# Performance work log

Measured on AMD Instinct MI355X. Metric: run time of the kernel, lower is better.

## Reference

```python
import jax, jax.numpy as jnp
import numpy as np

T, B, I, H, L = 512, 64, 1024, 1024, 2


def setup_inputs() -> dict:
    key = jax.random.key(0)
    ks = jax.random.split(key, 3)
    stdv = 1.0 / np.sqrt(H)
    x = jax.random.normal(ks[0], (T, B, I), dtype=jnp.float32)
    w_ih = jax.random.uniform(ks[1], (L, 4 * H, I), dtype=jnp.float32, minval=-stdv, maxval=stdv)
    w_hh = jax.random.uniform(ks[2], (L, 4 * H, H), dtype=jnp.float32, minval=-stdv, maxval=stdv)
    b_ih = jnp.zeros((L, 4 * H), dtype=jnp.float32)
    b_hh = jnp.zeros((L, 4 * H), dtype=jnp.float32)
    h0 = jnp.zeros((L, B, H), dtype=jnp.float32)
    c0 = jnp.zeros((L, B, H), dtype=jnp.float32)
    return {"x": x, "h0": h0, "c0": c0, "w_ih": w_ih, "w_hh": w_hh, "b_ih": b_ih, "b_hh": b_hh}


def _lstm_layer(seq, h, c, w_ih_l, w_hh_l, b_ih_l, b_hh_l):
    # in2hidden: one big GEMM over all timesteps, as in the torch code
    igates = jnp.einsum('tbi,gi->tbg', seq, w_ih_l) + b_ih_l  # (T, B, 4H)

    def step(carry, ig):
        h, c = carry
        gates = ig + h @ w_hh_l.T + b_hh_l          # (B, 4H)
        i_g, f_g, g_g, o_g = jnp.split(gates, 4, axis=-1)
        c = jax.nn.sigmoid(f_g) * c + jax.nn.sigmoid(i_g) * jnp.tanh(g_g)
        h = jax.nn.sigmoid(o_g) * jnp.tanh(c)
        return (h, c), h

    (hT, cT), out = jax.lax.scan(step, (h, c), igates)
    return out, hT, cT


def reference(x, h0, c0, w_ih, w_hh, b_ih, b_hh):
    out = x
    h_fin, c_fin = [], []
    for l in range(L):  # small fixed number of structurally distinct layers
        out, hT, cT = _lstm_layer(out, h0[l], c0[l], w_ih[l], w_hh[l], b_ih[l], b_hh[l])
        h_fin.append(hT)
        c_fin.append(cT)
    return out, jnp.stack(h_fin), jnp.stack(c_fin)
```

## Files before the change

### kernel.cpp

```cpp
#include <hip/hip_runtime.h>
#include <hip/hip_bf16.h>
#include <stdint.h>

#define T_STEPS 512
#define NBATCH 64
#define HID 1024
#define NGATE 4096
#define NLAYERS 2
#define BH (NBATCH * HID)
#define TBH (T_STEPS * NBATCH * HID)
#define WEL ((size_t)NLAYERS * NGATE * HID)
#define GBLK 128

typedef __attribute__((ext_vector_type(8))) short short8;
typedef __attribute__((ext_vector_type(4))) float f32x4;

__device__ __forceinline__ ushort f2bf(float f) {
  union { float f; uint32_t i; } u; u.f = f;
  return (ushort)((u.i + 0x7fffu + ((u.i >> 16) & 1u)) >> 16);
}
__device__ __forceinline__ void gll16(const void* g, void* l) {
  __builtin_amdgcn_global_load_lds(
      (const __attribute__((address_space(1))) unsigned int*)g,
      (__attribute__((address_space(3))) unsigned int*)l, 16, 0, 0);
}

#define ISSC(S, P, OFF) \
  asm volatile("global_load_dwordx4 %0, %1, off offset:" #OFF \
               : "=v"(fr[S]) : "v"(P));
#define VMW(N, SLOT) \
  asm volatile("s_waitcnt vmcnt(" #N ")" : "+v"(fr[SLOT]));
#define CON(SLOT, KC) { \
    const short8 b0v = *(const short8*)(bb0 + ((((KC) * 64) + kb) ^ bsw)); \
    const short8 b1v = *(const short8*)(bb1 + ((((KC) * 64) + kb) ^ bsw)); \
    accA = __builtin_amdgcn_mfma_f32_16x16x32_bf16(fr[SLOT], b0v, accA, 0, 0, 0); \
    accB = __builtin_amdgcn_mfma_f32_16x16x32_bf16(fr[SLOT], b1v, accB, 0, 0, 0); }

#define PIPE32(Pp, KB) \
  ISSC(0,Pp,0)    ISSC(1,Pp,64)   ISSC(2,Pp,128)  ISSC(3,Pp,192)  \
  ISSC(4,Pp,256)  ISSC(5,Pp,320)  ISSC(6,Pp,384)  ISSC(7,Pp,448)  \
  ISSC(8,Pp,512)  ISSC(9,Pp,576)  ISSC(10,Pp,640) ISSC(11,Pp,704) \
  ISSC(12,Pp,768) ISSC(13,Pp,832) ISSC(14,Pp,896) ISSC(15,Pp,960) \
  VMW(15,0)  CON(0,(KB)+0)   ISSC(0,Pp,1024)  \
  VMW(15,1)  CON(1,(KB)+1)   ISSC(1,Pp,1088)  \
  VMW(15,2)  CON(2,(KB)+2)   ISSC(2,Pp,1152)  \
  VMW(15,3)  CON(3,(KB)+3)   ISSC(3,Pp,1216)  \
  VMW(15,4)  CON(4,(KB)+4)   ISSC(4,Pp,1280)  \
  VMW(15,5)  CON(5,(KB)+5)   ISSC(5,Pp,1344)  \
  VMW(15,6)  CON(6,(KB)+6)   ISSC(6,Pp,1408)  \
  VMW(15,7)  CON(7,(KB)+7)   ISSC(7,Pp,1472)  \
  VMW(15,8)  CON(8,(KB)+8)   ISSC(8,Pp,1536)  \
  VMW(15,9)  CON(9,(KB)+9)   ISSC(9,Pp,1600)  \
  VMW(15,10) CON(10,(KB)+10) ISSC(10,Pp,1664) \
  VMW(15,11) CON(11,(KB)+11) ISSC(11,Pp,1728) \
  VMW(15,12) CON(12,(KB)+12) ISSC(12,Pp,1792) \
  VMW(15,13) CON(13,(KB)+13) ISSC(13,Pp,1856) \
  VMW(15,14) CON(14,(KB)+14) ISSC(14,Pp,1920) \
  VMW(15,15) CON(15,(KB)+15) ISSC(15,Pp,1984) \
  VMW(15,0)  CON(0,(KB)+16)  \
  VMW(14,1)  CON(1,(KB)+17)  \
  VMW(13,2)  CON(2,(KB)+18)  \
  VMW(12,3)  CON(3,(KB)+19)  \
  VMW(11,4)  CON(4,(KB)+20)  \
  VMW(10,5)  CON(5,(KB)+21)  \
  VMW(9,6)   CON(6,(KB)+22)  \
  VMW(8,7)   CON(7,(KB)+23)  \
  VMW(7,8)   CON(8,(KB)+24)  \
  VMW(6,9)   CON(9,(KB)+25)  \
  VMW(5,10)  CON(10,(KB)+26) \
  VMW(4,11)  CON(11,(KB)+27) \
  VMW(3,12)  CON(12,(KB)+28) \
  VMW(2,13)  CON(13,(KB)+29) \
  VMW(1,14)  CON(14,(KB)+30) \
  VMW(0,15)  CON(15,(KB)+31)

__global__ void k_f32_to_bf16(const float* __restrict__ in, ushort* __restrict__ out, int n) {
  int i = (blockIdx.x * blockDim.x + threadIdx.x) * 4;
  if (i >= n) return;
  const float4 v = *reinterpret_cast<const float4*>(in + i);
  ushort4 o; o.x = f2bf(v.x); o.y = f2bf(v.y); o.z = f2bf(v.z); o.w = f2bf(v.w);
  *reinterpret_cast<ushort4*>(out + i) = o;
}
__global__ void k_zero(int* p, int n) {
  int i = blockIdx.x * blockDim.x + threadIdx.x;
  if (i < n) p[i] = 0;
}

struct ScanP {
  const ushort* wih; const ushort* whh;
  const ushort* xb;  const ushort* hinit;
  ushort* h0r;
  ushort* h1r;
  const float* c0; const float* bi; const float* bh;
  float* out; int* bar;
};

__device__ __forceinline__ void garrive(int* gb, int stripe) {
  __syncthreads();
  if (threadIdx.x == 0)
    __hip_atomic_fetch_add(gb + stripe * 16, 1, __ATOMIC_RELAXED, __HIP_MEMORY_SCOPE_AGENT);
}
__device__ __forceinline__ void gwait(int* gb, int target, bool isRoot) {
  if (threadIdx.x == 0) {
    if (isRoot) {
      const int need = target * GBLK;
      for (;;) {
        int sum = 0;
#pragma unroll
        for (int i = 0; i < 16; ++i)
          sum += __hip_atomic_load(gb + i * 16, __ATOMIC_RELAXED, __HIP_MEMORY_SCOPE_AGENT);
        if (sum >= need) break;
        __builtin_amdgcn_s_sleep(1);
      }
      __hip_atomic_store(gb + 256, target, __ATOMIC_RELAXED, __HIP_MEMORY_SCOPE_AGENT);
    } else {
      while (__hip_atomic_load(gb + 256, __ATOMIC_RELAXED, __HIP_MEMORY_SCOPE_AGENT) < target)
        __builtin_amdgcn_s_sleep(2);
    }
  }
  __syncthreads();
  __builtin_amdgcn_sched_barrier(0);
}

__global__ __launch_bounds__(256, 1) void k_scan(ScanP p) {
  __shared__ __align__(16) ushort Wl[32 * 2048];
  __shared__ float glds[64 * 33];
  const int tid = threadIdx.x, wave = tid >> 6, lane = tid & 63;
  const bool isL1 = blockIdx.x >= 128;
  const int cb = isL1 ? (int)blockIdx.x - 128 : (int)blockIdx.x;
  const int j0 = cb * 8;
  const int stripe = cb & 15;
  const bool isRoot = (cb == 0);
  int* gb = p.bar + (isL1 ? 512 : 0);
  int* rel0 = p.bar + 256;

  const ushort* wihL = p.wih + (isL1 ? (size_t)NGATE * HID : 0);
  const ushort* whhL = p.whh + (isL1 ? (size_t)NGATE * HID : 0);
  for (int q = wave; q < 128; q += 4) {
    const int i = q >> 2, ch = q & 3;
    const ushort* base = (ch < 2) ? wihL : whhL;
    const int g = (i >> 3) * 1024 + j0 + (i & 7);
    gll16(base + (size_t)g * 1024 + (ch & 1) * 512 + (((lane * 16) ^ ((i & 7) << 4)) >> 1),
          (char*)Wl + i * 4096 + ch * 1024);
  }

  const int eb  = tid >> 2;
  const int jl0 = (tid & 3) * 2;
  const int jj  = j0 + jl0;
  const int lofs = isL1 ? NGATE : 0;
  float creg[2], bias[4][2];
#pragma unroll
  for (int i = 0; i < 2; ++i) creg[i] = p.c0[(isL1 ? BH : 0) + eb * 1024 + jj + i];
#pragma unroll
  for (int g = 0; g < 4; ++g)
#pragma unroll
    for (int i = 0; i < 2; ++i)
      bias[g][i] = p.bi[lofs + g * 1024 + jj + i] + p.bh[lofs + g * 1024 + jj + i];

  const size_t aoff = (size_t)(wave * 16 + (lane & 15)) * 1024 + (size_t)((lane >> 4) * 8);
  const int r0 = lane & 15;
  const char* bb0 = (const char*)Wl + r0 * 4096;
  const char* bb1 = (const char*)Wl + (r0 + 16) * 4096;
  const int bsw = (r0 & 7) << 4;
  const int kb = (lane >> 4) * 16;

  int seen0 = 0;

  __syncthreads();

  for (int t = 0; t < T_STEPS; ++t) {
    f32x4 accA = {0.f, 0.f, 0.f, 0.f}, accB = {0.f, 0.f, 0.f, 0.f};
    short8 fr[16];

    if (!isL1) {
      { const ushort* Pp = p.xb + (size_t)t * BH + aoff;
        PIPE32(Pp, 0) }
      if (t > 0) gwait(gb, t, isRoot);
      { const ushort* Qp = ((t == 0) ? p.hinit
                                     : p.h0r + (size_t)(t - 1) * BH) + aoff;
        PIPE32(Qp, 32) }
    } else {
      if (threadIdx.x == 0 && seen0 < t + 1) {
        int v = __hip_atomic_load(rel0, __ATOMIC_RELAXED, __HIP_MEMORY_SCOPE_AGENT);
        while (v < t + 1) {
          __builtin_amdgcn_s_sleep(2);
          v = __hip_atomic_load(rel0, __ATOMIC_RELAXED, __HIP_MEMORY_SCOPE_AGENT);
        }
        seen0 = v;
      }
      __syncthreads();
      __builtin_amdgcn_sched_barrier(0);
      { const ushort* Pp = p.h0r + (size_t)t * BH + aoff;
        PIPE32(Pp, 0) }
      if (t > 0) gwait(gb, t, isRoot);
      { const ushort* Qp = ((t == 0) ? p.hinit + BH
                                     : p.h1r + (size_t)(t - 1) * BH) + aoff;
        PIPE32(Qp, 32) }
    }

#pragma unroll
    for (int r = 0; r < 4; ++r) {
      const int row = wave * 16 + (lane >> 4) * 4 + r;
      glds[row * 33 + r0]      = accA[r];
      glds[row * 33 + 16 + r0] = accB[r];
    }
    __syncthreads();

    float hres[2];
#pragma unroll
    for (int i = 0; i < 2; ++i) {
      const int jl = jl0 + i;
      const float gi = glds[eb * 33 + jl]      + bias[0][i];
      const float gf = glds[eb * 33 + 8 + jl]  + bias[1][i];
      const float gg = glds[eb * 33 + 16 + jl] + bias[2][i];
      const float go = glds[eb * 33 + 24 + jl] + bias[3][i];
      float c = creg[i];
      const float si = 1.f / (1.f + __expf(-gi));
      const float sf = 1.f / (1.f + __expf(-gf));
      const float so = 1.f / (1.f + __expf(-go));
      const float tg = tanhf(gg);
      c = sf * c + si * tg;
      hres[i] = so * tanhf(c);
      creg[i] = c;
    }

    const uint32_t packed = (uint32_t)f2bf(hres[0]) | ((uint32_t)f2bf(hres[1]) << 16);
    ushort* hdst = (!isL1) ? (p.h0r + (size_t)t * BH) : (p.h1r + (size_t)t * BH);
    uint32_t* hw = (uint32_t*)(hdst + eb * 1024 + jj);
    __hip_atomic_store(hw, packed, __ATOMIC_RELAXED, __HIP_MEMORY_SCOPE_AGENT);
    uint32_t chk = __hip_atomic_load(hw, __ATOMIC_RELAXED, __HIP_MEMORY_SCOPE_AGENT);
    asm volatile("" :: "v"(chk));

    if (isL1) {
#pragma unroll
      for (int i = 0; i < 2; ++i)
        p.out[(size_t)t * BH + eb * 1024 + jj + i] = hres[i];
      if (t == T_STEPS - 1) {
#pragma unroll
        for (int i = 0; i < 2; ++i) {
          p.out[(size_t)TBH + BH + eb * 1024 + jj + i] = hres[i];
          p.out[(size_t)TBH + 3 * BH + eb * 1024 + jj + i] = creg[i];
        }
      }
    } else if (t == T_STEPS - 1) {
#pragma unroll
      for (int i = 0; i < 2; ++i) {
        p.out[(size_t)TBH + eb * 1024 + jj + i] = hres[i];
        p.out[(size_t)TBH + 2 * BH + eb * 1024 + jj + i] = creg[i];
      }
    }

    garrive(gb, stripe);
  }

  if (!isL1 && isRoot && threadIdx.x == 0) {
    const int need = T_STEPS * GBLK;
    for (;;) {
      int sum = 0;
#pragma unroll
      for (int i = 0; i < 16; ++i)
        sum += __hip_atomic_load(gb + i * 16, __ATOMIC_RELAXED, __HIP_MEMORY_SCOPE_AGENT);
      if (sum >= need) break;
      __builtin_amdgcn_s_sleep(1);
    }
    __hip_atomic_store(gb + 256, T_STEPS + 1, __ATOMIC_RELAXED, __HIP_MEMORY_SCOPE_AGENT);
  }
}

extern "C" void kernel_launch(void* const* d_in, const int* in_sizes, int n_in,
                              void* d_out, int out_size, void* d_ws, size_t ws_size,
                              hipStream_t stream) {
  const float* x    = (const float*)d_in[0];
  const float* h0   = (const float*)d_in[1];
  const float* c0   = (const float*)d_in[2];
  const float* w_ih = (const float*)d_in[3];
  const float* w_hh = (const float*)d_in[4];
  const float* b_ih = (const float*)d_in[5];
  const float* b_hh = (const float*)d_in[6];
  float* out = (float*)d_out;

  ushort* xb    = (ushort*)d_ws;
  ushort* wihb  = xb + (size_t)TBH;
  ushort* whhb  = wihb + WEL;
  ushort* hinit = whhb + WEL;
  ushort* h0r   = hinit + 2 * (size_t)BH;
  ushort* h1r   = h0r + (size_t)TBH;
  int*    bar   = (int*)(h1r + (size_t)TBH);

  const size_t need = ((size_t)3 * TBH + 2 * WEL + 2 * (size_t)BH) * 2 + 4096;
  if (ws_size < need) return;

  { int n = TBH;        k_f32_to_bf16<<<(n / 4 + 255) / 256, 256, 0, stream>>>(x, xb, n); }
  { int n = (int)WEL;   k_f32_to_bf16<<<(n / 4 + 255) / 256, 256, 0, stream>>>(w_ih, wihb, n); }
  { int n = (int)WEL;   k_f32_to_bf16<<<(n / 4 + 255) / 256, 256, 0, stream>>>(w_hh, whhb, n); }
  { int n = 2 * BH;     k_f32_to_bf16<<<(n / 4 + 255) / 256, 256, 0, stream>>>(h0, hinit, n); }
  k_zero<<<4, 256, 0, stream>>>(bar, 1024);

  ScanP sp;
  sp.wih = wihb; sp.whh = whhb;
  sp.xb = xb; sp.hinit = hinit;
  sp.h0r = h0r; sp.h1r = h1r;
  sp.c0 = c0; sp.bi = b_ih; sp.bh = b_hh;
  sp.out = out; sp.bar = bar;

  void* kp[1] = {&sp};
  hipLaunchCooperativeKernel(reinterpret_cast<void*>(&k_scan),
                             dim3(256), dim3(256), kp, 0, stream);
}
```

Measured before the change: 5.552 ms.

## Stream A-operand through LDS ring with global_load_lds instead of register prefetch

Replaces the 16-slot register prefetch of the activation operand (direct global_load_dwordx4 into VGPRs) with a 3-deep LDS ring buffer filled by global_load_lds. Each wave stages swizzled 16-row chunks into LDS and reads its MFMA operands back with ds_reads. The gate scratch area is aliased onto the same buffer, so a barrier is added before the gate writes. The aim is to cut VGPR pressure and issue wider, more coalesced loads. In exchange there is extra LDS traffic and a shallower prefetch depth on a latency-bound recurrent step.

Measured after the change: 7.658 ms. 37.9% more time.

```diff
diff --git a/kernel.cpp b/kernel.cpp
--- a/kernel.cpp
+++ b/kernel.cpp
@@ -25,54 +25,37 @@
       (__attribute__((address_space(3))) unsigned int*)l, 16, 0, 0);
 }
 
-#define ISSC(S, P, OFF) \
-  asm volatile("global_load_dwordx4 %0, %1, off offset:" #OFF \
-               : "=v"(fr[S]) : "v"(P));
-#define VMW(N, SLOT) \
-  asm volatile("s_waitcnt vmcnt(" #N ")" : "+v"(fr[SLOT]));
-#define CON(SLOT, KC) { \
-    const short8 b0v = *(const short8*)(bb0 + ((((KC) * 64) + kb) ^ bsw)); \
-    const short8 b1v = *(const short8*)(bb1 + ((((KC) * 64) + kb) ^ bsw)); \
-    accA = __builtin_amdgcn_mfma_f32_16x16x32_bf16(fr[SLOT], b0v, accA, 0, 0, 0); \
-    accB = __builtin_amdgcn_mfma_f32_16x16x32_bf16(fr[SLOT], b1v, accB, 0, 0, 0); }
-
-#define PIPE32(Pp, KB) \
-  ISSC(0,Pp,0)    ISSC(1,Pp,64)   ISSC(2,Pp,128)  ISSC(3,Pp,192)  \
-  ISSC(4,Pp,256)  ISSC(5,Pp,320)  ISSC(6,Pp,384)  ISSC(7,Pp,448)  \
-  ISSC(8,Pp,512)  ISSC(9,Pp,576)  ISSC(10,Pp,640) ISSC(11,Pp,704) \
-  ISSC(12,Pp,768) ISSC(13,Pp,832) ISSC(14,Pp,896) ISSC(15,Pp,960) \
-  VMW(15,0)  CON(0,(KB)+0)   ISSC(0,Pp,1024)  \
-  VMW(15,1)  CON(1,(KB)+1)   ISSC(1,Pp,1088)  \
-  VMW(15,2)  CON(2,(KB)+2)   ISSC(2,Pp,1152)  \
-  VMW(15,3)  CON(3,(KB)+3)   ISSC(3,Pp,1216)  \
-  VMW(15,4)  CON(4,(KB)+4)   ISSC(4,Pp,1280)  \
-  VMW(15,5)  CON(5,(KB)+5)   ISSC(5,Pp,1344)  \
-  VMW(15,6)  CON(6,(KB)+6)   ISSC(6,Pp,1408)  \
-  VMW(15,7)  CON(7,(KB)+7)   ISSC(7,Pp,1472)  \
-  VMW(15,8)  CON(8,(KB)+8)   ISSC(8,Pp,1536)  \
-  VMW(15,9)  CON(9,(KB)+9)   ISSC(9,Pp,1600)  \
-  VMW(15,10) CON(10,(KB)+10) ISSC(10,Pp,1664) \
-  VMW(15,11) CON(11,(KB)+11) ISSC(11,Pp,1728) \
-  VMW(15,12) CON(12,(KB)+12) ISSC(12,Pp,1792) \
-  VMW(15,13) CON(13,(KB)+13) ISSC(13,Pp,1856) \
-  VMW(15,14) CON(14,(KB)+14) ISSC(14,Pp,1920) \
-  VMW(15,15) CON(15,(KB)+15) ISSC(15,Pp,1984) \
-  VMW(15,0)  CON(0,(KB)+16)  \
-  VMW(14,1)  CON(1,(KB)+17)  \
-  VMW(13,2)  CON(2,(KB)+18)  \
-  VMW(12,3)  CON(3,(KB)+19)  \
-  VMW(11,4)  CON(4,(KB)+20)  \
-  VMW(10,5)  CON(5,(KB)+21)  \
-  VMW(9,6)   CON(6,(KB)+22)  \
-  VMW(8,7)   CON(7,(KB)+23)  \
-  VMW(7,8)   CON(8,(KB)+24)  \
-  VMW(6,9)   CON(9,(KB)+25)  \
-  VMW(5,10)  CON(10,(KB)+26) \
-  VMW(4,11)  CON(11,(KB)+27) \
-  VMW(3,12)  CON(12,(KB)+28) \
-  VMW(2,13)  CON(13,(KB)+29) \
-  VMW(1,14)  CON(14,(KB)+30) \
-  VMW(0,15)  CON(15,(KB)+31)
+#define STAGE(C, Sp) \
+  gll16(Sp + aoffs0 + (C) * 64, AbD + ((C) % 3) * 8192); \
+  gll16(Sp + aoffs1 + (C) * 64, AbD + ((C) % 3) * 8192 + 1024);
+#define GW(N) { asm volatile("s_waitcnt vmcnt(" #N ")" ::: "memory"); \
+                __builtin_amdgcn_sched_barrier(0); }
+#define CONL(C, S, KB) { \
+  const short8 av  = *(const short8*)(AbR + ((C) % 3) * 8192 + ((((S) * 64) + kb4) ^ asw)); \
+  const short8 b0v = *(const short8*)(bb0 + ((((KB) + (C) * 2 + (S)) * 64 + kb) ^ bsw)); \
+  const short8 b1v = *(const short8*)(bb1 + ((((KB) + (C) * 2 + (S)) * 64 + kb) ^ bsw)); \
+  accA = __builtin_amdgcn_mfma_f32_16x16x32_bf16(av, b0v, accA, 0, 0, 0); \
+  accB = __builtin_amdgcn_mfma_f32_16x16x32_bf16(av, b1v, accB, 0, 0, 0); }
+#define CONSUME(C, KB) CONL(C, 0, KB) CONL(C, 1, KB)
+
+#define HALF(Sp, KB) \
+  STAGE(0,Sp) STAGE(1,Sp) STAGE(2,Sp) \
+  GW(4) CONSUME(0,(KB))  STAGE(3,Sp)  \
+  GW(4) CONSUME(1,(KB))  STAGE(4,Sp)  \
+  GW(4) CONSUME(2,(KB))  STAGE(5,Sp)  \
+  GW(4) CONSUME(3,(KB))  STAGE(6,Sp)  \
+  GW(4) CONSUME(4,(KB))  STAGE(7,Sp)  \
+  GW(4) CONSUME(5,(KB))  STAGE(8,Sp)  \
+  GW(4) CONSUME(6,(KB))  STAGE(9,Sp)  \
+  GW(4) CONSUME(7,(KB))  STAGE(10,Sp) \
+  GW(4) CONSUME(8,(KB))  STAGE(11,Sp) \
+  GW(4) CONSUME(9,(KB))  STAGE(12,Sp) \
+  GW(4) CONSUME(10,(KB)) STAGE(13,Sp) \
+  GW(4) CONSUME(11,(KB)) STAGE(14,Sp) \
+  GW(4) CONSUME(12,(KB)) STAGE(15,Sp) \
+  GW(4) CONSUME(13,(KB)) \
+  GW(2) CONSUME(14,(KB)) \
+  GW(0) CONSUME(15,(KB))
 
 __global__ void k_f32_to_bf16(const float* __restrict__ in, ushort* __restrict__ out, int n) {
   int i = (blockIdx.x * blockDim.x + threadIdx.x) * 4;
@@ -124,7 +107,8 @@
 
 __global__ __launch_bounds__(256, 1) void k_scan(ScanP p) {
   __shared__ __align__(16) ushort Wl[32 * 2048];
-  __shared__ float glds[64 * 33];
+  __shared__ __align__(16) char Abuf[3 * 8192];
+  float* glds = (float*)Abuf;
   const int tid = threadIdx.x, wave = tid >> 6, lane = tid & 63;
   const bool isL1 = blockIdx.x >= 128;
   const int cb = isL1 ? (int)blockIdx.x - 128 : (int)blockIdx.x;
@@ -132,7 +116,7 @@
   const int stripe = cb & 15;
   const bool isRoot = (cb == 0);
   int* gb = p.bar + (isL1 ? 512 : 0);
-  int* rel0 = p.bar + 256;
+  const int* rel0 = p.bar + 256;
 
   const ushort* wihL = p.wih + (isL1 ? (size_t)NGATE * HID : 0);
   const ushort* whhL = p.whh + (isL1 ? (size_t)NGATE * HID : 0);
@@ -157,7 +141,15 @@
     for (int i = 0; i < 2; ++i)
       bias[g][i] = p.bi[lofs + g * 1024 + jj + i] + p.bh[lofs + g * 1024 + jj + i];
 
-  const size_t aoff = (size_t)(wave * 16 + (lane & 15)) * 1024 + (size_t)((lane >> 4) * 8);
+  const int rowq = lane >> 3;
+  const int swb  = ((lane & 7) * 16) ^ (rowq << 4);
+  const size_t aoffs0 = (size_t)(wave * 16 + rowq) * 1024 + (swb >> 1);
+  const size_t aoffs1 = (size_t)(wave * 16 + 8 + rowq) * 1024 + (swb >> 1);
+  char* AbD = Abuf + wave * 2048;
+  const int arow = wave * 16 + (lane & 15);
+  const char* AbR = Abuf + arow * 128;
+  const int asw = (lane & 7) << 4;
+  const int kb4 = (lane >> 4) * 16;
   const int r0 = lane & 15;
   const char* bb0 = (const char*)Wl + r0 * 4096;
   const char* bb1 = (const char*)Wl + (r0 + 16) * 4096;
@@ -170,15 +162,13 @@
 
   for (int t = 0; t < T_STEPS; ++t) {
     f32x4 accA = {0.f, 0.f, 0.f, 0.f}, accB = {0.f, 0.f, 0.f, 0.f};
-    short8 fr[16];
 
     if (!isL1) {
-      { const ushort* Pp = p.xb + (size_t)t * BH + aoff;
-        PIPE32(Pp, 0) }
+      { const ushort* Sp = p.xb + (size_t)t * BH;
+        HALF(Sp, 0) }
       if (t > 0) gwait(gb, t, isRoot);
-      { const ushort* Qp = ((t == 0) ? p.hinit
-                                     : p.h0r + (size_t)(t - 1) * BH) + aoff;
-        PIPE32(Qp, 32) }
+      { const ushort* Sp = (t == 0) ? p.hinit : p.h0r + (size_t)(t - 1) * BH;
+        HALF(Sp, 32) }
     } else {
       if (threadIdx.x == 0 && seen0 < t + 1) {
         int v = __hip_atomic_load(rel0, __ATOMIC_RELAXED, __HIP_MEMORY_SCOPE_AGENT);
@@ -190,13 +180,14 @@
       }
       __syncthreads();
       __builtin_amdgcn_sched_barrier(0);
-      { const ushort* Pp = p.h0r + (size_t)t * BH + aoff;
-        PIPE32(Pp, 0) }
+      { const ushort* Sp = p.h0r + (size_t)t * BH;
+        HALF(Sp, 0) }
       if (t > 0) gwait(gb, t, isRoot);
-      { const ushort* Qp = ((t == 0) ? p.hinit + BH
-                                     : p.h1r + (size_t)(t - 1) * BH) + aoff;
-        PIPE32(Qp, 32) }
-    }
+      { const ushort* Sp = (t == 0) ? p.hinit + BH : p.h1r + (size_t)(t - 1) * BH;
+        HALF(Sp, 32) }
+    }
+
+    __syncthreads();
 
 #pragma unroll
     for (int r = 0; r < 4; ++r) {
```
